# Optimization experiments

Hardware: AMD Instinct MI355X
Metric: run time of the kernel (lower is better)

The kernel has to match this reference:

```python
import jax, jax.numpy as jnp
import numpy as np

N = 500000
D = 112
H = 64
W = 176


def setup_inputs() -> dict:
    key = jax.random.key(0)
    k1, k2 = jax.random.split(key)
    # positions: x in [0, W-1), y in [0, H-1)
    u = jax.random.uniform(k1, (N, 2), dtype=jnp.float32)
    sampling_positions = u * jnp.array([W - 1.0, H - 1.0], dtype=jnp.float32)
    sampling_depth_features = jax.random.normal(k2, (N, D), dtype=jnp.float32)
    return {
        "sampling_positions": sampling_positions,
        "sampling_depth_features": sampling_depth_features,
        "height": H,
        "width": W,
    }


def _bilinear_scatter(positions, features, height, width):
    # positions: [N,2] (x, y); features: [N,D] -> grid [H,W,D]
    x = positions[:, 0]
    y = positions[:, 1]
    x0 = jnp.floor(x)
    y0 = jnp.floor(y)
    wx = x - x0
    wy = y - y0
    x0i = x0.astype(jnp.int32)
    y0i = y0.astype(jnp.int32)
    x1i = x0i + 1
    y1i = y0i + 1

    out = jnp.zeros((height, width, features.shape[1]), dtype=jnp.float32)

    def in_bounds(yi, xi):
        return (yi >= 0) & (yi < height) & (xi >= 0) & (xi < width)

    corners = [
        (y0i, x0i, (1.0 - wy) * (1.0 - wx)),
        (y0i, x1i, (1.0 - wy) * wx),
        (y1i, x0i, wy * (1.0 - wx)),
        (y1i, x1i, wy * wx),
    ]
    for yi, xi, w in corners:
        valid = in_bounds(yi, xi)
        w = jnp.where(valid, w, 0.0)
        yi = jnp.clip(yi, 0, height - 1)
        xi = jnp.clip(xi, 0, width - 1)
        out = out.at[yi, xi].add(w[:, None] * features)
    return out


def reference(sampling_positions, sampling_depth_features, height, width):
    return _bilinear_scatter(sampling_positions, sampling_depth_features, height, width)
```

## Files before the change

kernel.cpp:

```cpp
#include <hip/hip_runtime.h>


#define D     112
#define D2    56
#define H     64
#define W     176
#define HW    (H * W)
#define S     2
#define SCAP  64
#define CSTR  16
#define TY    4
#define TX    4
#define GX    (W / TX)
#define GY    (H / TY)
#define NCELL (TY * TX)
#define NW    8

__device__ __forceinline__ void fill_one(int p, float x, float y,
                                         int* cnt, uint2* bucket)
{
    float xf = floorf(x), yf = floorf(y);
    float wx = x - xf,    wy = y - yf;
    int x0 = min(max((int)xf, 0), W - 1);
    int y0 = min(max((int)yf, 0), H - 1);
    int sb = (y0 * W + x0) * S + (p & 1);
    unsigned qw = (__float2uint_rn(wy * 65535.0f) << 16)
                |  __float2uint_rn(wx * 65535.0f);
    int i = atomicAdd(&cnt[sb * CSTR], 1);
    if (i < SCAP) bucket[(size_t)sb * SCAP + i] = make_uint2((unsigned)p, qw);
}

__global__ __launch_bounds__(256) void fill_kernel(
    const float4* __restrict__ pos2,
    int* __restrict__ cnt,
    uint2* __restrict__ bucket,
    int N)
{
    int i = blockIdx.x * blockDim.x + threadIdx.x;
    int p0 = 2 * i;
    if (p0 >= N) return;
    if (p0 + 1 < N) {
        float4 q = pos2[i];
        fill_one(p0,     q.x, q.y, cnt, bucket);
        fill_one(p0 + 1, q.z, q.w, cnt, bucket);
    } else {
        float2 q = ((const float2*)pos2)[p0];
        fill_one(p0, q.x, q.y, cnt, bucket);
    }
}

__global__ __launch_bounds__(512, 6) void accum_kernel(
    const float* __restrict__ feat,
    const int* __restrict__ cnt,
    const uint2* __restrict__ bucket,
    float* __restrict__ out)
{
    const int tile = blockIdx.x;
    const int ty0  = (tile / GX) * TY;
    const int tx0  = (tile % GX) * TX;
    const int t    = threadIdx.x;
    const int wid  = t >> 6;
    const int lane = t & 63;
    const bool act = lane < D2;

    float2 acc[NCELL];
#pragma unroll
    for (int c = 0; c < NCELL; ++c) acc[c] = make_float2(0.0f, 0.0f);

#pragma unroll
    for (int by = -1; by < TY; ++by) {
#pragma unroll
        for (int bx = -1; bx < TX; ++bx) {
            const int gby = ty0 + by;
            const int gbx = tx0 + bx;
            if (gby < 0 || gbx < 0 || gbx >= W) continue;
            const int bin = gby * W + gbx;
#pragma unroll
            for (int s = 0; s < S; ++s) {
                const int sb = bin * S + s;
                const int n  = min(cnt[sb * CSTR], SCAP);
                const uint2* __restrict__ bk = bucket + (size_t)sb * SCAP;
#pragma unroll 2
                for (int e = wid; e < n; e += NW) {
                    uint2 en = bk[e];
                    float wx = (float)(en.y & 0xffffu) * (1.0f / 65535.0f);
                    float wy = (float)(en.y >> 16)     * (1.0f / 65535.0f);
                    float2 f = make_float2(0.0f, 0.0f);
                    if (act)
                        f = ((const float2*)(feat + (size_t)en.x * D))[lane];
                    float ax = 1.0f - wx, ay = 1.0f - wy;
#pragma unroll
                    for (int dy = 0; dy < 2; ++dy) {
                        const int cy = by + dy;
                        if (cy < 0 || cy >= TY) continue;
                        const float fy = dy ? wy : ay;
#pragma unroll
                        for (int dx = 0; dx < 2; ++dx) {
                            const int cx = bx + dx;
                            if (cx < 0 || cx >= TX) continue;
                            const float fw = fy * (dx ? wx : ax);
                            const int c = cy * TX + cx;
                            acc[c].x = fmaf(fw, f.x, acc[c].x);
                            acc[c].y = fmaf(fw, f.y, acc[c].y);
                        }
                    }
                }
            }
        }
    }

    __shared__ float2 sacc[2][NCELL][D2];
    const int half = wid >> 2;
    const int sub  = wid & 3;

    for (int w = 0; w < 4; ++w) {
        if (sub == w && act) {
            if (w == 0) {
#pragma unroll
                for (int c = 0; c < NCELL; ++c) sacc[half][c][lane] = acc[c];
            } else {
#pragma unroll
                for (int c = 0; c < NCELL; ++c) {
                    float2 v = sacc[half][c][lane];
                    v.x += acc[c].x; v.y += acc[c].y;
                    sacc[half][c][lane] = v;
                }
            }
        }
        __syncthreads();
    }

    if (act) {
#pragma unroll
        for (int k = 0; k < 2; ++k) {
            const int c  = wid * 2 + k;
            const int cy = c / TX, cx = c % TX;
            float2 v0 = sacc[0][c][lane];
            float2 v1 = sacc[1][c][lane];
            float2* dst = (float2*)(out + ((size_t)(ty0 + cy) * W + (tx0 + cx)) * D);
            dst[lane] = make_float2(v0.x + v1.x, v0.y + v1.y);
        }
    }
}

extern "C" void kernel_launch(void* const* d_in, const int* in_sizes, int n_in,
                              void* d_out, int out_size, void* d_ws, size_t ws_size,
                              hipStream_t stream) {
    const float4* pos2 = (const float4*)d_in[0];
    const float* feat  = (const float*)d_in[1];
    float* out         = (float*)d_out;

    const int N = in_sizes[0] / 2;

    int* cnt      = (int*)d_ws;
    uint2* bucket = (uint2*)((char*)d_ws + (size_t)HW * S * CSTR * sizeof(int));

    hipMemsetAsync(cnt, 0, (size_t)HW * S * CSTR * sizeof(int), stream);

    int npair = (N + 1) / 2;
    fill_kernel<<<(npair + 255) / 256, 256, 0, stream>>>(pos2, cnt, bucket, N);

    accum_kernel<<<GY * GX, 512, 0, stream>>>(feat, cnt, bucket, out);
}
```

Before: 426.5 us.

## Merge bin sub-buckets and assign whole bins to warps with 4-way batched loads

```diff
diff --git a/kernel.cpp b/kernel.cpp
--- a/kernel.cpp
+++ b/kernel.cpp
@@ -6,8 +6,7 @@
 #define H     64
 #define W     176
 #define HW    (H * W)
-#define S     2
-#define SCAP  64
+#define CAP   128
 #define CSTR  16
 #define TY    4
 #define TX    4
@@ -23,11 +22,11 @@
     float wx = x - xf,    wy = y - yf;
     int x0 = min(max((int)xf, 0), W - 1);
     int y0 = min(max((int)yf, 0), H - 1);
-    int sb = (y0 * W + x0) * S + (p & 1);
+    int bin = y0 * W + x0;
     unsigned qw = (__float2uint_rn(wy * 65535.0f) << 16)
                 |  __float2uint_rn(wx * 65535.0f);
-    int i = atomicAdd(&cnt[sb * CSTR], 1);
-    if (i < SCAP) bucket[(size_t)sb * SCAP + i] = make_uint2((unsigned)p, qw);
+    int i = atomicAdd(&cnt[bin * CSTR], 1);
+    if (i < CAP) bucket[(size_t)bin * CAP + i] = make_uint2((unsigned)p, qw);
 }
 
 __global__ __launch_bounds__(256) void fill_kernel(
@@ -71,40 +70,53 @@
     for (int by = -1; by < TY; ++by) {
 #pragma unroll
         for (int bx = -1; bx < TX; ++bx) {
+            const int binLin = (by + 1) * 5 + (bx + 1);
+            if ((binLin & 7) != wid) continue;
             const int gby = ty0 + by;
             const int gbx = tx0 + bx;
             if (gby < 0 || gbx < 0 || gbx >= W) continue;
-            const int bin = gby * W + gbx;
+
+            const int n = min(cnt[(gby * W + gbx) * CSTR], CAP);
+            const uint2* __restrict__ bk =
+                bucket + (size_t)(gby * W + gbx) * CAP;
+
+            auto proc = [&](uint2 en, float2 f) {
+                float wx = (float)(en.y & 0xffffu) * (1.0f / 65535.0f);
+                float wy = (float)(en.y >> 16)     * (1.0f / 65535.0f);
+                float ax = 1.0f - wx, ay = 1.0f - wy;
 #pragma unroll
-            for (int s = 0; s < S; ++s) {
-                const int sb = bin * S + s;
-                const int n  = min(cnt[sb * CSTR], SCAP);
-                const uint2* __restrict__ bk = bucket + (size_t)sb * SCAP;
-#pragma unroll 2
-                for (int e = wid; e < n; e += NW) {
-                    uint2 en = bk[e];
-                    float wx = (float)(en.y & 0xffffu) * (1.0f / 65535.0f);
-                    float wy = (float)(en.y >> 16)     * (1.0f / 65535.0f);
-                    float2 f = make_float2(0.0f, 0.0f);
-                    if (act)
-                        f = ((const float2*)(feat + (size_t)en.x * D))[lane];
-                    float ax = 1.0f - wx, ay = 1.0f - wy;
+                for (int dy = 0; dy < 2; ++dy) {
+                    const int cy = by + dy;
+                    if (cy < 0 || cy >= TY) continue;
+                    const float fy = dy ? wy : ay;
 #pragma unroll
-                    for (int dy = 0; dy < 2; ++dy) {
-                        const int cy = by + dy;
-                        if (cy < 0 || cy >= TY) continue;
-                        const float fy = dy ? wy : ay;
-#pragma unroll
-                        for (int dx = 0; dx < 2; ++dx) {
-                            const int cx = bx + dx;
-                            if (cx < 0 || cx >= TX) continue;
-                            const float fw = fy * (dx ? wx : ax);
-                            const int c = cy * TX + cx;
-                            acc[c].x = fmaf(fw, f.x, acc[c].x);
-                            acc[c].y = fmaf(fw, f.y, acc[c].y);
-                        }
+                    for (int dx = 0; dx < 2; ++dx) {
+                        const int cx = bx + dx;
+                        if (cx < 0 || cx >= TX) continue;
+                        const float fw = fy * (dx ? wx : ax);
+                        const int c = cy * TX + cx;
+                        acc[c].x = fmaf(fw, f.x, acc[c].x);
+                        acc[c].y = fmaf(fw, f.y, acc[c].y);
                     }
                 }
+            };
+            auto ldrow = [&](unsigned p) -> float2 {
+                return act ? ((const float2*)(feat + (size_t)p * D))[lane]
+                           : make_float2(0.0f, 0.0f);
+            };
+
+            int e = 0;
+            for (; e + 4 <= n; e += 4) {
+                uint2 n0 = bk[e], n1 = bk[e + 1], n2 = bk[e + 2], n3 = bk[e + 3];
+                float2 f0 = ldrow(n0.x);
+                float2 f1 = ldrow(n1.x);
+                float2 f2 = ldrow(n2.x);
+                float2 f3 = ldrow(n3.x);
+                proc(n0, f0); proc(n1, f1); proc(n2, f2); proc(n3, f3);
+            }
+            for (; e < n; ++e) {
+                uint2 n0 = bk[e];
+                proc(n0, ldrow(n0.x));
             }
         }
     }
@@ -153,9 +165,9 @@
     const int N = in_sizes[0] / 2;
 
     int* cnt      = (int*)d_ws;
-    uint2* bucket = (uint2*)((char*)d_ws + (size_t)HW * S * CSTR * sizeof(int));
+    uint2* bucket = (uint2*)((char*)d_ws + (size_t)HW * CSTR * sizeof(int));
 
-    hipMemsetAsync(cnt, 0, (size_t)HW * S * CSTR * sizeof(int), stream);
+    hipMemsetAsync(cnt, 0, (size_t)HW * CSTR * sizeof(int), stream);
 
     int npair = (N + 1) / 2;
     fill_kernel<<<(npair + 255) / 256, 256, 0, stream>>>(pos2, cnt, bucket, N);
```

New measurement: 364.1 us. 14.6% less time.

## Stage tile bucket headers in LDS with single sub-bucket and contiguous wave splits

Applied to the files above, without the earlier changes.

```diff
diff --git a/kernel.cpp b/kernel.cpp
--- a/kernel.cpp
+++ b/kernel.cpp
@@ -6,8 +6,7 @@
 #define H     64
 #define W     176
 #define HW    (H * W)
-#define S     2
-#define SCAP  64
+#define CAP   128
 #define CSTR  16
 #define TY    4
 #define TX    4
@@ -15,6 +14,8 @@
 #define GY    (H / TY)
 #define NCELL (TY * TX)
 #define NW    8
+#define NBIN  25
+#define NSLOT (NBIN * CAP)
 
 __device__ __forceinline__ void fill_one(int p, float x, float y,
                                          int* cnt, uint2* bucket)
@@ -23,29 +24,35 @@
     float wx = x - xf,    wy = y - yf;
     int x0 = min(max((int)xf, 0), W - 1);
     int y0 = min(max((int)yf, 0), H - 1);
-    int sb = (y0 * W + x0) * S + (p & 1);
+    int bin = y0 * W + x0;
     unsigned qw = (__float2uint_rn(wy * 65535.0f) << 16)
                 |  __float2uint_rn(wx * 65535.0f);
-    int i = atomicAdd(&cnt[sb * CSTR], 1);
-    if (i < SCAP) bucket[(size_t)sb * SCAP + i] = make_uint2((unsigned)p, qw);
+    int i = atomicAdd(&cnt[bin * CSTR], 1);
+    if (i < CAP) bucket[(size_t)bin * CAP + i] = make_uint2((unsigned)p, qw);
 }
 
 __global__ __launch_bounds__(256) void fill_kernel(
-    const float4* __restrict__ pos2,
+    const float2* __restrict__ pos,
     int* __restrict__ cnt,
     uint2* __restrict__ bucket,
     int N)
 {
     int i = blockIdx.x * blockDim.x + threadIdx.x;
-    int p0 = 2 * i;
+    int p0 = 4 * i;
     if (p0 >= N) return;
-    if (p0 + 1 < N) {
-        float4 q = pos2[i];
-        fill_one(p0,     q.x, q.y, cnt, bucket);
-        fill_one(p0 + 1, q.z, q.w, cnt, bucket);
+    const float4* p4 = (const float4*)pos;
+    if (p0 + 3 < N) {
+        float4 a = p4[2 * i];
+        float4 b = p4[2 * i + 1];
+        fill_one(p0,     a.x, a.y, cnt, bucket);
+        fill_one(p0 + 1, a.z, a.w, cnt, bucket);
+        fill_one(p0 + 2, b.x, b.y, cnt, bucket);
+        fill_one(p0 + 3, b.z, b.w, cnt, bucket);
     } else {
-        float2 q = ((const float2*)pos2)[p0];
-        fill_one(p0, q.x, q.y, cnt, bucket);
+        for (int k = 0; k < 4 && p0 + k < N; ++k) {
+            float2 q = pos[p0 + k];
+            fill_one(p0 + k, q.x, q.y, cnt, bucket);
+        }
     }
 }
 
@@ -63,6 +70,30 @@
     const int lane = t & 63;
     const bool act = lane < D2;
 
+    __shared__ int sn[NBIN];
+    __shared__ __align__(16) char smem[NSLOT * sizeof(uint2)];
+    uint2* shdr = (uint2*)smem;
+
+    if (t < NBIN) {
+        int by = t / 5 - 1, bx = t % 5 - 1;
+        int gby = ty0 + by, gbx = tx0 + bx;
+        int n = 0;
+        if (gby >= 0 && gbx >= 0 && gbx < W)
+            n = min(cnt[(gby * W + gbx) * CSTR], CAP);
+        sn[t] = n;
+    }
+    __syncthreads();
+
+    for (int i = t; i < NSLOT; i += 512) {
+        int b = i >> 7, s = i & (CAP - 1);
+        if (s < sn[b]) {
+            int by = b / 5 - 1, bx = b % 5 - 1;
+            int gbin = (ty0 + by) * W + (tx0 + bx);
+            shdr[i] = bucket[(size_t)gbin * CAP + s];
+        }
+    }
+    __syncthreads();
+
     float2 acc[NCELL];
 #pragma unroll
     for (int c = 0; c < NCELL; ++c) acc[c] = make_float2(0.0f, 0.0f);
@@ -71,45 +102,42 @@
     for (int by = -1; by < TY; ++by) {
 #pragma unroll
         for (int bx = -1; bx < TX; ++bx) {
-            const int gby = ty0 + by;
-            const int gbx = tx0 + bx;
-            if (gby < 0 || gbx < 0 || gbx >= W) continue;
-            const int bin = gby * W + gbx;
+            const int b  = (by + 1) * 5 + (bx + 1);
+            const int n  = sn[b];
+            const int lo = (n * wid) >> 3;
+            const int hi = (n * (wid + 1)) >> 3;
+            const uint2* hb = shdr + b * CAP;
+
+#pragma unroll 4
+            for (int e = lo; e < hi; ++e) {
+                uint2 en = hb[e];
+                float wx = (float)(en.y & 0xffffu) * (1.0f / 65535.0f);
+                float wy = (float)(en.y >> 16)     * (1.0f / 65535.0f);
+                float2 f = make_float2(0.0f, 0.0f);
+                if (act)
+                    f = ((const float2*)(feat + (size_t)en.x * D))[lane];
+                float ax = 1.0f - wx, ay = 1.0f - wy;
 #pragma unroll
-            for (int s = 0; s < S; ++s) {
-                const int sb = bin * S + s;
-                const int n  = min(cnt[sb * CSTR], SCAP);
-                const uint2* __restrict__ bk = bucket + (size_t)sb * SCAP;
-#pragma unroll 2
-                for (int e = wid; e < n; e += NW) {
-                    uint2 en = bk[e];
-                    float wx = (float)(en.y & 0xffffu) * (1.0f / 65535.0f);
-                    float wy = (float)(en.y >> 16)     * (1.0f / 65535.0f);
-                    float2 f = make_float2(0.0f, 0.0f);
-                    if (act)
-                        f = ((const float2*)(feat + (size_t)en.x * D))[lane];
-                    float ax = 1.0f - wx, ay = 1.0f - wy;
+                for (int dy = 0; dy < 2; ++dy) {
+                    const int cy = by + dy;
+                    if (cy < 0 || cy >= TY) continue;
+                    const float fy = dy ? wy : ay;
 #pragma unroll
-                    for (int dy = 0; dy < 2; ++dy) {
-                        const int cy = by + dy;
-                        if (cy < 0 || cy >= TY) continue;
-                        const float fy = dy ? wy : ay;
-#pragma unroll
-                        for (int dx = 0; dx < 2; ++dx) {
-                            const int cx = bx + dx;
-                            if (cx < 0 || cx >= TX) continue;
-                            const float fw = fy * (dx ? wx : ax);
-                            const int c = cy * TX + cx;
-                            acc[c].x = fmaf(fw, f.x, acc[c].x);
-                            acc[c].y = fmaf(fw, f.y, acc[c].y);
-                        }
+                    for (int dx = 0; dx < 2; ++dx) {
+                        const int cx = bx + dx;
+                        if (cx < 0 || cx >= TX) continue;
+                        const float fw = fy * (dx ? wx : ax);
+                        const int c = cy * TX + cx;
+                        acc[c].x = fmaf(fw, f.x, acc[c].x);
+                        acc[c].y = fmaf(fw, f.y, acc[c].y);
                     }
                 }
             }
         }
     }
 
-    __shared__ float2 sacc[2][NCELL][D2];
+    __syncthreads();
+    float2 (*sacc)[NCELL][D2] = reinterpret_cast<float2 (*)[NCELL][D2]>(smem);
     const int half = wid >> 2;
     const int sub  = wid & 3;
 
@@ -146,19 +174,19 @@
 extern "C" void kernel_launch(void* const* d_in, const int* in_sizes, int n_in,
                               void* d_out, int out_size, void* d_ws, size_t ws_size,
                               hipStream_t stream) {
-    const float4* pos2 = (const float4*)d_in[0];
-    const float* feat  = (const float*)d_in[1];
-    float* out         = (float*)d_out;
+    const float2* pos = (const float2*)d_in[0];
+    const float* feat = (const float*)d_in[1];
+    float* out        = (float*)d_out;
 
     const int N = in_sizes[0] / 2;
 
     int* cnt      = (int*)d_ws;
-    uint2* bucket = (uint2*)((char*)d_ws + (size_t)HW * S * CSTR * sizeof(int));
+    uint2* bucket = (uint2*)((char*)d_ws + (size_t)HW * CSTR * sizeof(int));
 
-    hipMemsetAsync(cnt, 0, (size_t)HW * S * CSTR * sizeof(int), stream);
+    hipMemsetAsync(cnt, 0, (size_t)HW * CSTR * sizeof(int), stream);
 
-    int npair = (N + 1) / 2;
-    fill_kernel<<<(npair + 255) / 256, 256, 0, stream>>>(pos2, cnt, bucket, N);
+    int nq = (N + 3) / 4;
+    fill_kernel<<<(nq + 255) / 256, 256, 0, stream>>>(pos, cnt, bucket, N);
 
     accum_kernel<<<GY * GX, 512, 0, stream>>>(feat, cnt, bucket, out);
 }
```

After: 364.2 us. 1.17x faster.
